# Performance work log

Measured on AMD Instinct MI355X. Metric: run time of the kernel, lower is better.

Reference implementation:

```python
import jax, jax.numpy as jnp
import numpy as np

H = 1024  # hidden_dim

def setup_inputs() -> dict:
    key = jax.random.key(0)
    ks = jax.random.split(key, 6)
    B, T, D = 4096, 28, 28
    x = jax.random.normal(ks[0], (B, T, D), dtype=jnp.float32)
    key_seq = jax.random.normal(ks[1], (8, T, D), dtype=jnp.float32)
    s_ih = 1.0 / np.sqrt(D)
    s_hh = 1.0 / np.sqrt(H)
    W_ih = jax.random.normal(ks[2], (D, 4 * H), dtype=jnp.float32) * s_ih
    W_hh = jax.random.normal(ks[3], (H, 4 * H), dtype=jnp.float32) * s_hh
    b = jnp.zeros((4 * H,), dtype=jnp.float32)
    W_cls = jax.random.normal(ks[4], (H, 10), dtype=jnp.float32) * s_hh
    b_cls = jnp.zeros((10,), dtype=jnp.float32)
    return {"x": x, "key_seq": key_seq, "W_ih": W_ih, "W_hh": W_hh,
            "b": b, "W_cls": W_cls, "b_cls": b_cls}


def _lstm_last(xs, h0, c0, W_ih, W_hh, b):
    """Run LSTM over xs [B,T,D]; return final (h, c), each [B,H]."""
    xs_t = jnp.swapaxes(xs, 0, 1)  # [T,B,D]

    def step(carry, xt):
        h, c = carry
        g = xt @ W_ih + h @ W_hh + b  # [B,4H]
        i, f, gg, o = jnp.split(g, 4, axis=-1)
        c = jax.nn.sigmoid(f) * c + jax.nn.sigmoid(i) * jnp.tanh(gg)
        h = jax.nn.sigmoid(o) * jnp.tanh(c)
        return (h, c), None

    (h, c), _ = jax.lax.scan(step, (h0, c0), xs_t)
    return h, c


def reference(x, key_seq, W_ih, W_hh, b, W_cls, b_cls):
    B = x.shape[0]
    Kb = key_seq.shape[0]
    zk = jnp.zeros((Kb, H), dtype=x.dtype)
    # key modulation: run the key sequences through the same recurrence;
    # the mean final state seeds the initial state for the data pass.
    hk, ck = _lstm_last(key_seq, zk, zk, W_ih, W_hh, b)
    h0 = jnp.broadcast_to(hk.mean(axis=0), (B, H))
    c0 = jnp.broadcast_to(ck.mean(axis=0), (B, H))
    h, _ = _lstm_last(x, h0, c0, W_ih, W_hh, b)
    # dropout is identity in eval mode
    return h @ W_cls + b_cls  # [B,10]
```

## Files before the change

### kernel.cpp

```cpp
#include <hip/hip_runtime.h>
#include <hip/hip_bf16.h>
#include <stdint.h>

#define HID 1024
#define G4H 4096
#define BATCH 4096
#define TSTEPS 28
#define DIN 28
#define KTOT 1056
#define NKEY 8
#define NTILES 33

typedef __attribute__((ext_vector_type(8))) __bf16 b16x8;
typedef __attribute__((ext_vector_type(4))) __bf16 b16x4;
typedef __attribute__((ext_vector_type(4))) float f32x4;
typedef __attribute__((address_space(1))) unsigned int u32_g;
typedef __attribute__((address_space(3))) unsigned int u32_l;

__device__ __forceinline__ void async16(const __hip_bfloat16* g, __hip_bfloat16* l) {
  __builtin_amdgcn_global_load_lds((u32_g*)g, (u32_l*)l, 16, 0, 0);
}

__device__ __forceinline__ float sigmoidf_(float x) { return 1.f / (1.f + __expf(-x)); }
__device__ __forceinline__ float tanhfast_(float x) { return 2.f / (1.f + __expf(-2.f * x)) - 1.f; }

__device__ __forceinline__ int nprime(int gate, int j) {
  return ((j >> 4) << 6) + (gate << 4) + (j & 15);
}

__global__ __launch_bounds__(256) void prep_weights(
    const float* __restrict__ W_hh, const float* __restrict__ W_ih,
    __hip_bfloat16* __restrict__ Wt, float* __restrict__ kstate) {
  __shared__ float tile[64][65];
  const int k0 = blockIdx.x * 64, n0 = blockIdx.y * 64;
  const int tid = threadIdx.x;
  const int fid = (blockIdx.y * gridDim.x + blockIdx.x) * 256 + tid;
  if (fid < 2 * NKEY * HID) kstate[fid] = 0.f;
  for (int i = tid; i < 4096; i += 256) {
    int kk = i >> 6, nn = i & 63;
    int k = k0 + kk;
    float v = 0.f;
    if (k < HID) v = W_hh[k * G4H + n0 + nn];
    else if (k < HID + DIN) v = W_ih[(k - HID) * G4H + n0 + nn];
    tile[kk][nn] = v;
  }
  __syncthreads();
  for (int i = tid; i < 4096; i += 256) {
    int nn = i >> 6, kk = i & 63;
    int k = k0 + kk;
    int n = n0 + nn;
    int np = nprime(n >> 10, n & 1023);
    if (k < KTOT) Wt[(size_t)np * KTOT + k] = __float2bfloat16(tile[kk][nn]);
  }
}

__global__ __launch_bounds__(256) void key_step(
    const __hip_bfloat16* __restrict__ Wt, const float* __restrict__ key_seq,
    const float* __restrict__ bias, const float* __restrict__ hk_in,
    float* __restrict__ hk_out, float* __restrict__ ck, int t) {
  __shared__ float sh[NKEY][KTOT];
  __shared__ float sred[32][8][8];
  const int tid = threadIdx.x;
#pragma unroll
  for (int key = 0; key < NKEY; ++key)
    for (int k = tid; k < HID; k += 256) sh[key][k] = hk_in[key * HID + k];
  for (int i = tid; i < NKEY * 32; i += 256) {
    int key = i >> 5, d = i & 31;
    sh[key][HID + d] = (d < DIN) ? key_seq[key * (TSTEPS * DIN) + t * DIN + d] : 0.f;
  }
  __syncthreads();
  const int rowIdx = tid >> 3;
  const int kpart = tid & 7;
  const int gate = rowIdx >> 3, jj = rowIdx & 7;
  const int j0 = blockIdx.x * 8;
  const int np = nprime(gate, j0 + jj);
  const __hip_bfloat16* wrow = Wt + (size_t)np * KTOT + kpart * 132;
  const int kb = kpart * 132;
  float acc[NKEY];
#pragma unroll
  for (int key = 0; key < NKEY; ++key) acc[key] = 0.f;
  for (int kk = 0; kk < 132; kk += 4) {
    b16x4 wv = *(const b16x4*)(wrow + kk);
    float w0 = (float)wv[0], w1 = (float)wv[1], w2 = (float)wv[2], w3 = (float)wv[3];
#pragma unroll
    for (int key = 0; key < NKEY; ++key) {
      const float* s = &sh[key][kb + kk];
      acc[key] += w0 * s[0] + w1 * s[1] + w2 * s[2] + w3 * s[3];
    }
  }
#pragma unroll
  for (int key = 0; key < NKEY; ++key) sred[rowIdx][kpart][key] = acc[key];
  __syncthreads();
  if (tid < 64) {
    int key = tid >> 3, j2 = tid & 7;
    float g[4];
#pragma unroll
    for (int gg = 0; gg < 4; ++gg) {
      float s = 0.f;
#pragma unroll
      for (int p = 0; p < 8; ++p) s += sred[gg * 8 + j2][p][key];
      g[gg] = s + bias[gg * HID + j0 + j2];
    }
    size_t ci = (size_t)key * HID + j0 + j2;
    float cv = sigmoidf_(g[1]) * ck[ci] + sigmoidf_(g[0]) * tanhfast_(g[2]);
    ck[ci] = cv;
    hk_out[ci] = sigmoidf_(g[3]) * tanhfast_(cv);
  }
}

__global__ __launch_bounds__(256) void key_mean(
    const float* __restrict__ hk, const float* __restrict__ ck,
    float* __restrict__ h0, float* __restrict__ c0) {
  int j = blockIdx.x * 256 + threadIdx.x;
  float sh_ = 0.f, sc_ = 0.f;
#pragma unroll
  for (int k = 0; k < NKEY; ++k) { sh_ += hk[k * HID + j]; sc_ += ck[k * HID + j]; }
  h0[j] = sh_ * (1.f / NKEY);
  c0[j] = sc_ * (1.f / NKEY);
}

__global__ __launch_bounds__(256) void main_init(
    const float* __restrict__ h0, const float* __restrict__ c0,
    const float* __restrict__ x, __hip_bfloat16* __restrict__ A0,
    __hip_bfloat16* __restrict__ A1, float* __restrict__ c) {
  int idx = blockIdx.x * 256 + threadIdx.x;
  int b = idx / KTOT, col = idx - b * KTOT;
  if (col < HID) {
    A0[idx] = __float2bfloat16(h0[col]);
    c[b * HID + col] = c0[col];
  } else if (col < HID + DIN) {
    A0[idx] = __float2bfloat16(x[b * (TSTEPS * DIN) + (col - HID)]);
  } else {
    A0[idx] = __float2bfloat16(0.f);
    A1[idx] = __float2bfloat16(0.f);
  }
}

__global__ __launch_bounds__(512, 1) void gemm_lstm(
    const __hip_bfloat16* __restrict__ Ain, const __hip_bfloat16* __restrict__ Wt,
    const float* __restrict__ bias, float* __restrict__ cst,
    __hip_bfloat16* __restrict__ Aout, const float* __restrict__ x,
    float* __restrict__ hfin, int tstep) {
  __shared__ alignas(16) __hip_bfloat16 sA[4][256 * 32];
  __shared__ alignas(16) __hip_bfloat16 sB[4][256 * 32];
  const int tid = threadIdx.x;
  const int lane = tid & 63, wave = tid >> 6;
  const int wr = wave >> 2, wc = wave & 3;
  const int jt = blockIdx.x, mt = blockIdx.y;
  const int brow = mt * 256;
  const int lrow = lane & 15, kq = lane >> 4;
  const int sx = (lrow >> 1) & 3;

  const int strow = tid >> 2;
  const int sslot = (tid & 3) ^ ((tid >> 3) & 3);
  const __hip_bfloat16* gA = Ain + (size_t)(brow + strow) * KTOT + sslot * 8;
  const __hip_bfloat16* gB = Wt + (size_t)(jt * 256 + strow) * KTOT + sslot * 8;
  const size_t rstep = (size_t)128 * KTOT;

  int iA[8], iB[4];
#pragma unroll
  for (int m = 0; m < 8; ++m) iA[m] = (wr * 128 + m * 16 + lrow) * 4 + (kq ^ sx);
#pragma unroll
  for (int g = 0; g < 4; ++g) iB[g] = (wc * 64 + g * 16 + lrow) * 4 + (kq ^ sx);

  f32x4 acc[8][4] = {};

#define STAGE(base, dst, kt) do { \
    async16((base) + (size_t)(kt) * 32, (dst) + tid * 8); \
    async16((base) + rstep + (size_t)(kt) * 32, (dst) + 4096 + tid * 8); \
  } while (0)

  STAGE(gA, sA[0], 0); STAGE(gB, sB[0], 0);
  STAGE(gA, sA[1], 1); STAGE(gB, sB[1], 1);
  asm volatile("s_waitcnt vmcnt(4)" ::: "memory");
  __builtin_amdgcn_s_barrier();

#pragma unroll 1
  for (int t = 0; t < NTILES; ++t) {
    const b16x8* cA = (const b16x8*)sA[t & 3];
    const b16x8* cB = (const b16x8*)sB[t & 3];
    __hip_bfloat16* pA = sA[(t + 2) & 3];
    __hip_bfloat16* pB = sB[(t + 2) & 3];
    b16x8 af[4], bf[4];
    if (t < NTILES - 2) STAGE(gA, pA, t + 2);
#pragma unroll
    for (int m = 0; m < 4; ++m) af[m] = cA[iA[m]];
#pragma unroll
    for (int g = 0; g < 4; ++g) bf[g] = cB[iB[g]];
    __builtin_amdgcn_s_barrier();
    __builtin_amdgcn_s_setprio(1);
#pragma unroll
    for (int g = 0; g < 4; ++g)
#pragma unroll
      for (int m = 0; m < 4; ++m)
        acc[m][g] = __builtin_amdgcn_mfma_f32_16x16x32_bf16(af[m], bf[g], acc[m][g], 0, 0, 0);
    __builtin_amdgcn_s_setprio(0);
    __builtin_amdgcn_s_barrier();
    if (t < NTILES - 2) STAGE(gB, pB, t + 2);
#pragma unroll
    for (int m = 0; m < 4; ++m) af[m] = cA[iA[m + 4]];
    if (t < NTILES - 2) asm volatile("s_waitcnt vmcnt(4)" ::: "memory");
    else if (t == NTILES - 2) asm volatile("s_waitcnt vmcnt(0)" ::: "memory");
    __builtin_amdgcn_s_barrier();
    __builtin_amdgcn_s_setprio(1);
#pragma unroll
    for (int g = 0; g < 4; ++g)
#pragma unroll
      for (int m = 0; m < 4; ++m)
        acc[m + 4][g] = __builtin_amdgcn_mfma_f32_16x16x32_bf16(af[m], bf[g], acc[m + 4][g], 0, 0, 0);
    __builtin_amdgcn_s_setprio(0);
    __builtin_amdgcn_s_barrier();
  }
#undef STAGE

  const int j = jt * 64 + wc * 16 + lrow;
  const float b_i = bias[j], b_f = bias[HID + j];
  const float b_g = bias[2 * HID + j], b_o = bias[3 * HID + j];
#pragma unroll
  for (int m = 0; m < 8; ++m) {
    const int row0 = brow + wr * 128 + m * 16 + kq * 4;
#pragma unroll
    for (int r = 0; r < 4; ++r) {
      const int row = row0 + r;
      const size_t ci = (size_t)row * HID + j;
      float gi = acc[m][0][r] + b_i;
      float gf = acc[m][1][r] + b_f;
      float gg = acc[m][2][r] + b_g;
      float go = acc[m][3][r] + b_o;
      float cv = sigmoidf_(gf) * cst[ci] + sigmoidf_(gi) * tanhfast_(gg);
      cst[ci] = cv;
      float h = sigmoidf_(go) * tanhfast_(cv);
      Aout[(size_t)row * KTOT + j] = __float2bfloat16(h);
      if (tstep == TSTEPS - 1) hfin[ci] = h;
    }
  }
  if (jt == 0 && tstep + 1 < TSTEPS) {
    for (int i = tid; i < 256 * DIN; i += 512) {
      int rr = i / DIN, d = i - rr * DIN;
      Aout[(size_t)(brow + rr) * KTOT + HID + d] =
          __float2bfloat16(x[(size_t)(brow + rr) * (TSTEPS * DIN) + (tstep + 1) * DIN + d]);
    }
  }
}

__global__ __launch_bounds__(256) void classifier(
    const float* __restrict__ hfin, const float* __restrict__ W_cls,
    const float* __restrict__ b_cls, float* __restrict__ out) {
  __shared__ float sw[HID * 10];
  __shared__ float sred[10][257];
  const int b = blockIdx.x, tid = threadIdx.x;
  for (int i = tid; i < HID * 10; i += 256) sw[i] = W_cls[i];
  __syncthreads();
  float acc[10];
#pragma unroll
  for (int cls = 0; cls < 10; ++cls) acc[cls] = 0.f;
  for (int j = tid; j < HID; j += 256) {
    float hv = hfin[(size_t)b * HID + j];
#pragma unroll
    for (int cls = 0; cls < 10; ++cls) acc[cls] += hv * sw[j * 10 + cls];
  }
#pragma unroll
  for (int cls = 0; cls < 10; ++cls) sred[cls][tid] = acc[cls];
  __syncthreads();
  for (int off = 128; off > 0; off >>= 1) {
    if (tid < off)
#pragma unroll
      for (int cls = 0; cls < 10; ++cls) sred[cls][tid] += sred[cls][tid + off];
    __syncthreads();
  }
  if (tid < 10) out[b * 10 + tid] = sred[tid][0] + b_cls[tid];
}

extern "C" void kernel_launch(void* const* d_in, const int* in_sizes, int n_in,
                              void* d_out, int out_size, void* d_ws, size_t ws_size,
                              hipStream_t stream) {
  const float* x      = (const float*)d_in[0];
  const float* keyseq = (const float*)d_in[1];
  const float* W_ih   = (const float*)d_in[2];
  const float* W_hh   = (const float*)d_in[3];
  const float* bias   = (const float*)d_in[4];
  const float* W_cls  = (const float*)d_in[5];
  const float* b_cls  = (const float*)d_in[6];
  float* out = (float*)d_out;
  (void)in_sizes; (void)n_in; (void)out_size; (void)ws_size;

  char* p = (char*)d_ws;
  auto alloc = [&](size_t bytes) { char* r = p; p += (bytes + 255) & ~(size_t)255; return r; };
  __hip_bfloat16* Wt = (__hip_bfloat16*)alloc((size_t)G4H * KTOT * 2);
  __hip_bfloat16* A0 = (__hip_bfloat16*)alloc((size_t)BATCH * KTOT * 2);
  __hip_bfloat16* A1 = (__hip_bfloat16*)alloc((size_t)BATCH * KTOT * 2);
  float* c    = (float*)alloc((size_t)BATCH * HID * 4);
  float* hfin = (float*)alloc((size_t)BATCH * HID * 4);
  float* hk0  = (float*)alloc((size_t)NKEY * HID * 4);
  float* ck   = (float*)alloc((size_t)NKEY * HID * 4);
  float* hk1  = (float*)alloc((size_t)NKEY * HID * 4);
  float* h0   = (float*)alloc((size_t)HID * 4);
  float* c0   = (float*)alloc((size_t)HID * 4);

  prep_weights<<<dim3(17, 64), 256, 0, stream>>>(W_hh, W_ih, Wt, hk0);

  float* kbuf[2] = {hk0, hk1};
  for (int t = 0; t < TSTEPS; ++t)
    key_step<<<128, 256, 0, stream>>>(Wt, keyseq, bias, kbuf[t & 1], kbuf[(t + 1) & 1], ck, t);
  key_mean<<<4, 256, 0, stream>>>(hk0, ck, h0, c0);

  main_init<<<(BATCH * KTOT) / 256, 256, 0, stream>>>(h0, c0, x, A0, A1, c);

  __hip_bfloat16* Ab[2] = {A0, A1};
  for (int t = 0; t < TSTEPS; ++t)
    gemm_lstm<<<dim3(16, 16), 512, 0, stream>>>(Ab[t & 1], Wt, bias, c,
                                                Ab[(t + 1) & 1], x, hfin, t);
  classifier<<<BATCH, 256, 0, stream>>>(hfin, W_cls, b_cls, out);
}
```

Measured before the change: 2.288 ms.

## Replace per-timestep GEMM launches with persistent LSTM kernel and grid barrier

Folds the 28 per-timestep gemm_lstm launches into one persistent kernel of 512 blocks at two blocks per CU. A software grid barrier built on an atomic counter separates timesteps. The cell state now stays in registers across steps instead of going through global memory. Hidden outputs are staged in LDS for vectorised stores, and the tiles are smaller (256x128) with double buffering instead of four-stage buffering. The goal is to remove launch overhead and the c-state memory traffic, at the cost of barrier spin latency, reliance on every block being co-resident, and a less deep pipeline.

```diff
diff --git a/kernel.cpp b/kernel.cpp
--- a/kernel.cpp
+++ b/kernel.cpp
@@ -10,6 +10,7 @@
 #define KTOT 1056
 #define NKEY 8
 #define NTILES 33
+#define NBLK 512
 
 typedef __attribute__((ext_vector_type(8))) __bf16 b16x8;
 typedef __attribute__((ext_vector_type(4))) __bf16 b16x4;
@@ -26,6 +27,21 @@
 
 __device__ __forceinline__ int nprime(int gate, int j) {
   return ((j >> 4) << 6) + (gate << 4) + (j & 15);
+}
+
+__device__ __forceinline__ void gridbar(unsigned* cnt, unsigned target) {
+  __threadfence();
+  __syncthreads();
+  if (threadIdx.x == 0) {
+    __hip_atomic_fetch_add(cnt, 1u, __ATOMIC_RELEASE, __HIP_MEMORY_SCOPE_AGENT);
+    unsigned v;
+    do {
+      __builtin_amdgcn_s_sleep(2);
+      v = __hip_atomic_load(cnt, __ATOMIC_ACQUIRE, __HIP_MEMORY_SCOPE_AGENT);
+    } while (v < target);
+  }
+  __syncthreads();
+  __threadfence();
 }
 
 __global__ __launch_bounds__(256) void prep_weights(
@@ -120,14 +136,12 @@
 }
 
 __global__ __launch_bounds__(256) void main_init(
-    const float* __restrict__ h0, const float* __restrict__ c0,
-    const float* __restrict__ x, __hip_bfloat16* __restrict__ A0,
-    __hip_bfloat16* __restrict__ A1, float* __restrict__ c) {
+    const float* __restrict__ h0, const float* __restrict__ x,
+    __hip_bfloat16* __restrict__ A0, __hip_bfloat16* __restrict__ A1) {
   int idx = blockIdx.x * 256 + threadIdx.x;
   int b = idx / KTOT, col = idx - b * KTOT;
   if (col < HID) {
     A0[idx] = __float2bfloat16(h0[col]);
-    c[b * HID + col] = c0[col];
   } else if (col < HID + DIN) {
     A0[idx] = __float2bfloat16(x[b * (TSTEPS * DIN) + (col - HID)]);
   } else {
@@ -136,110 +150,124 @@
   }
 }
 
-__global__ __launch_bounds__(512, 1) void gemm_lstm(
-    const __hip_bfloat16* __restrict__ Ain, const __hip_bfloat16* __restrict__ Wt,
-    const float* __restrict__ bias, float* __restrict__ cst,
-    __hip_bfloat16* __restrict__ Aout, const float* __restrict__ x,
-    float* __restrict__ hfin, int tstep) {
-  __shared__ alignas(16) __hip_bfloat16 sA[4][256 * 32];
-  __shared__ alignas(16) __hip_bfloat16 sB[4][256 * 32];
+__global__ __launch_bounds__(256, 2) void lstm_persist(
+    const __hip_bfloat16* __restrict__ Wt,
+    __hip_bfloat16* __restrict__ A0, __hip_bfloat16* __restrict__ A1,
+    const float* __restrict__ bias, const float* __restrict__ c0,
+    const float* __restrict__ x, float* __restrict__ hfin,
+    unsigned* __restrict__ barcnt) {
+  __shared__ alignas(16) __hip_bfloat16 sA[2][256 * 32];
+  __shared__ alignas(16) __hip_bfloat16 sB[2][128 * 32];
   const int tid = threadIdx.x;
   const int lane = tid & 63, wave = tid >> 6;
-  const int wr = wave >> 2, wc = wave & 3;
-  const int jt = blockIdx.x, mt = blockIdx.y;
+  const int wr = wave >> 1, wc = wave & 1;
+  const int bid = blockIdx.x;
+  const int q = bid >> 3;
+  const int mt = ((bid >> 2) & 1) * 8 + (q >> 3);
+  const int jt = (bid & 3) * 8 + (q & 7);
   const int brow = mt * 256;
   const int lrow = lane & 15, kq = lane >> 4;
   const int sx = (lrow >> 1) & 3;
 
-  const int strow = tid >> 2;
-  const int sslot = (tid & 3) ^ ((tid >> 3) & 3);
-  const __hip_bfloat16* gA = Ain + (size_t)(brow + strow) * KTOT + sslot * 8;
-  const __hip_bfloat16* gB = Wt + (size_t)(jt * 256 + strow) * KTOT + sslot * 8;
-  const size_t rstep = (size_t)128 * KTOT;
-
-  int iA[8], iB[4];
+  int aoff[4], boff[2];
+#pragma unroll
+  for (int r = 0; r < 4; ++r) {
+    int g = r * 256 + tid;
+    int row = g >> 2, slot = (g & 3) ^ ((g >> 3) & 3);
+    aoff[r] = (brow + row) * KTOT + slot * 8;
+  }
+#pragma unroll
+  for (int r = 0; r < 2; ++r) {
+    int g = r * 256 + tid;
+    int row = g >> 2, slot = (g & 3) ^ ((g >> 3) & 3);
+    boff[r] = (jt * 128 + row) * KTOT + slot * 8;
+  }
+  int iA[8], iB4[4];
 #pragma unroll
   for (int m = 0; m < 8; ++m) iA[m] = (wr * 128 + m * 16 + lrow) * 4 + (kq ^ sx);
 #pragma unroll
-  for (int g = 0; g < 4; ++g) iB[g] = (wc * 64 + g * 16 + lrow) * 4 + (kq ^ sx);
-
-  f32x4 acc[8][4] = {};
-
-#define STAGE(base, dst, kt) do { \
-    async16((base) + (size_t)(kt) * 32, (dst) + tid * 8); \
-    async16((base) + rstep + (size_t)(kt) * 32, (dst) + 4096 + tid * 8); \
-  } while (0)
-
-  STAGE(gA, sA[0], 0); STAGE(gB, sB[0], 0);
-  STAGE(gA, sA[1], 1); STAGE(gB, sB[1], 1);
-  asm volatile("s_waitcnt vmcnt(4)" ::: "memory");
-  __builtin_amdgcn_s_barrier();
-
-#pragma unroll 1
-  for (int t = 0; t < NTILES; ++t) {
-    const b16x8* cA = (const b16x8*)sA[t & 3];
-    const b16x8* cB = (const b16x8*)sB[t & 3];
-    __hip_bfloat16* pA = sA[(t + 2) & 3];
-    __hip_bfloat16* pB = sB[(t + 2) & 3];
-    b16x8 af[4], bf[4];
-    if (t < NTILES - 2) STAGE(gA, pA, t + 2);
-#pragma unroll
-    for (int m = 0; m < 4; ++m) af[m] = cA[iA[m]];
-#pragma unroll
-    for (int g = 0; g < 4; ++g) bf[g] = cB[iB[g]];
-    __builtin_amdgcn_s_barrier();
-    __builtin_amdgcn_s_setprio(1);
-#pragma unroll
-    for (int g = 0; g < 4; ++g)
-#pragma unroll
-      for (int m = 0; m < 4; ++m)
-        acc[m][g] = __builtin_amdgcn_mfma_f32_16x16x32_bf16(af[m], bf[g], acc[m][g], 0, 0, 0);
-    __builtin_amdgcn_s_setprio(0);
-    __builtin_amdgcn_s_barrier();
-    if (t < NTILES - 2) STAGE(gB, pB, t + 2);
-#pragma unroll
-    for (int m = 0; m < 4; ++m) af[m] = cA[iA[m + 4]];
-    if (t < NTILES - 2) asm volatile("s_waitcnt vmcnt(4)" ::: "memory");
-    else if (t == NTILES - 2) asm volatile("s_waitcnt vmcnt(0)" ::: "memory");
-    __builtin_amdgcn_s_barrier();
-    __builtin_amdgcn_s_setprio(1);
-#pragma unroll
-    for (int g = 0; g < 4; ++g)
-#pragma unroll
-      for (int m = 0; m < 4; ++m)
-        acc[m + 4][g] = __builtin_amdgcn_mfma_f32_16x16x32_bf16(af[m], bf[g], acc[m + 4][g], 0, 0, 0);
-    __builtin_amdgcn_s_setprio(0);
-    __builtin_amdgcn_s_barrier();
-  }
-#undef STAGE
-
-  const int j = jt * 64 + wc * 16 + lrow;
+  for (int g = 0; g < 4; ++g) iB4[g] = (wc * 64 + g * 16 + lrow) * 4 + (kq ^ sx);
+
+  const int j = jt * 32 + wc * 16 + lrow;
   const float b_i = bias[j], b_f = bias[HID + j];
   const float b_g = bias[2 * HID + j], b_o = bias[3 * HID + j];
-#pragma unroll
-  for (int m = 0; m < 8; ++m) {
-    const int row0 = brow + wr * 128 + m * 16 + kq * 4;
-#pragma unroll
-    for (int r = 0; r < 4; ++r) {
-      const int row = row0 + r;
-      const size_t ci = (size_t)row * HID + j;
-      float gi = acc[m][0][r] + b_i;
-      float gf = acc[m][1][r] + b_f;
-      float gg = acc[m][2][r] + b_g;
-      float go = acc[m][3][r] + b_o;
-      float cv = sigmoidf_(gf) * cst[ci] + sigmoidf_(gi) * tanhfast_(gg);
-      cst[ci] = cv;
-      float h = sigmoidf_(go) * tanhfast_(cv);
-      Aout[(size_t)row * KTOT + j] = __float2bfloat16(h);
-      if (tstep == TSTEPS - 1) hfin[ci] = h;
-    }
-  }
-  if (jt == 0 && tstep + 1 < TSTEPS) {
-    for (int i = tid; i < 256 * DIN; i += 512) {
-      int rr = i / DIN, d = i - rr * DIN;
-      Aout[(size_t)(brow + rr) * KTOT + HID + d] =
-          __float2bfloat16(x[(size_t)(brow + rr) * (TSTEPS * DIN) + (tstep + 1) * DIN + d]);
-    }
+  float cst[8][4];
+  const float cinit = c0[j];
+#pragma unroll
+  for (int m = 0; m < 8; ++m)
+#pragma unroll
+    for (int r = 0; r < 4; ++r) cst[m][r] = cinit;
+
+#pragma unroll 1
+  for (int s = 0; s < TSTEPS; ++s) {
+    const __hip_bfloat16* ain = (s & 1) ? A1 : A0;
+    __hip_bfloat16* aout = (s & 1) ? A0 : A1;
+    f32x4 acc[8][4] = {};
+
+#pragma unroll
+    for (int r = 0; r < 4; ++r) async16(ain + aoff[r], &sA[0][(r * 256 + tid) * 8]);
+#pragma unroll
+    for (int r = 0; r < 2; ++r) async16(Wt + boff[r], &sB[0][(r * 256 + tid) * 8]);
+    __syncthreads();
+
+#pragma unroll 1
+    for (int t = 0; t < NTILES; ++t) {
+      if (t < NTILES - 1) {
+        const int ko = (t + 1) * 32;
+        const int nb = (t + 1) & 1;
+#pragma unroll
+        for (int r = 0; r < 4; ++r) async16(ain + aoff[r] + ko, &sA[nb][(r * 256 + tid) * 8]);
+#pragma unroll
+        for (int r = 0; r < 2; ++r) async16(Wt + boff[r] + ko, &sB[nb][(r * 256 + tid) * 8]);
+      }
+      const b16x8* cA = (const b16x8*)sA[t & 1];
+      const b16x8* cB = (const b16x8*)sB[t & 1];
+      b16x8 bf[4];
+#pragma unroll
+      for (int g = 0; g < 4; ++g) bf[g] = cB[iB4[g]];
+      __builtin_amdgcn_s_setprio(1);
+#pragma unroll
+      for (int m = 0; m < 8; ++m) {
+        b16x8 af = cA[iA[m]];
+#pragma unroll
+        for (int g = 0; g < 4; ++g)
+          acc[m][g] = __builtin_amdgcn_mfma_f32_16x16x32_bf16(af, bf[g], acc[m][g], 0, 0, 0);
+      }
+      __builtin_amdgcn_s_setprio(0);
+      __syncthreads();
+    }
+
+    __hip_bfloat16* sH = &sA[0][0];
+#pragma unroll
+    for (int m = 0; m < 8; ++m)
+#pragma unroll
+      for (int r = 0; r < 4; ++r) {
+        float gi = acc[m][0][r] + b_i;
+        float gf = acc[m][1][r] + b_f;
+        float gg = acc[m][2][r] + b_g;
+        float go = acc[m][3][r] + b_o;
+        float cv = sigmoidf_(gf) * cst[m][r] + sigmoidf_(gi) * tanhfast_(gg);
+        cst[m][r] = cv;
+        float h = sigmoidf_(go) * tanhfast_(cv);
+        const int lr = wr * 128 + m * 16 + kq * 4 + r;
+        sH[lr * 32 + wc * 16 + lrow] = __float2bfloat16(h);
+        if (s == TSTEPS - 1) hfin[(size_t)(brow + lr) * HID + j] = h;
+      }
+    __syncthreads();
+    {
+      const b16x8* sHv = (const b16x8*)sH;
+      __hip_bfloat16* dst = aout + (size_t)(brow + tid) * KTOT + jt * 32;
+#pragma unroll
+      for (int qq = 0; qq < 4; ++qq)
+        *(b16x8*)(dst + qq * 8) = sHv[tid * 4 + qq];
+    }
+    if (jt == 0 && s + 1 < TSTEPS) {
+      const float* xr = x + (size_t)(brow + tid) * (TSTEPS * DIN) + (s + 1) * DIN;
+      __hip_bfloat16* ar = aout + (size_t)(brow + tid) * KTOT + HID;
+#pragma unroll
+      for (int d = 0; d < DIN; ++d) ar[d] = __float2bfloat16(xr[d]);
+    }
+    if (s + 1 < TSTEPS) gridbar(barcnt, (unsigned)(NBLK * (s + 1)));
   }
 }
 
@@ -289,13 +317,13 @@
   __hip_bfloat16* Wt = (__hip_bfloat16*)alloc((size_t)G4H * KTOT * 2);
   __hip_bfloat16* A0 = (__hip_bfloat16*)alloc((size_t)BATCH * KTOT * 2);
   __hip_bfloat16* A1 = (__hip_bfloat16*)alloc((size_t)BATCH * KTOT * 2);
-  float* c    = (float*)alloc((size_t)BATCH * HID * 4);
   float* hfin = (float*)alloc((size_t)BATCH * HID * 4);
   float* hk0  = (float*)alloc((size_t)NKEY * HID * 4);
   float* ck   = (float*)alloc((size_t)NKEY * HID * 4);
   float* hk1  = (float*)alloc((size_t)NKEY * HID * 4);
   float* h0   = (float*)alloc((size_t)HID * 4);
   float* c0   = (float*)alloc((size_t)HID * 4);
+  unsigned* barcnt = (unsigned*)alloc(256);
 
   prep_weights<<<dim3(17, 64), 256, 0, stream>>>(W_hh, W_ih, Wt, hk0);
 
@@ -304,11 +332,10 @@
     key_step<<<128, 256, 0, stream>>>(Wt, keyseq, bias, kbuf[t & 1], kbuf[(t + 1) & 1], ck, t);
   key_mean<<<4, 256, 0, stream>>>(hk0, ck, h0, c0);
 
-  main_init<<<(BATCH * KTOT) / 256, 256, 0, stream>>>(h0, c0, x, A0, A1, c);
-
-  __hip_bfloat16* Ab[2] = {A0, A1};
-  for (int t = 0; t < TSTEPS; ++t)
-    gemm_lstm<<<dim3(16, 16), 512, 0, stream>>>(Ab[t & 1], Wt, bias, c,
-                                                Ab[(t + 1) & 1], x, hfin, t);
+  main_init<<<(BATCH * KTOT) / 256, 256, 0, stream>>>(h0, x, A0, A1);
+  hipMemsetAsync(barcnt, 0, 256, stream);
+
+  lstm_persist<<<NBLK, 256, 0, stream>>>(Wt, A0, A1, bias, c0, x, hfin, barcnt);
+
   classifier<<<BATCH, 256, 0, stream>>>(hfin, W_cls, b_cls, out);
 }
```

Result: slower. 7.475 ms (+226.8%).
